# Performance work log

Measured on AMD Instinct MI355X. Metric: run time of the kernel, lower is better.

## Reference

```python
import jax, jax.numpy as jnp
import numpy as np

B = 8192; L = 68; NPG = L + 1; N = B * NPG
IN = 4; HID = 64; OUT = 7; NL = 8
BN_EPS = 1e-5


def setup_inputs() -> dict:
    key = jax.random.key(0)
    ks = jax.random.split(key, 12)
    # graph topology (same for every graph): ring among L landmarks + master node (idx L)
    # connected to every landmark; directed edges both ways (PyG-style edge_index).
    ring = np.stack([np.arange(L), (np.arange(L) + 1) % L])            # [2, L]
    mast = np.stack([np.arange(L), np.full(L, L)])                     # [2, L]
    und = np.concatenate([ring, mast], axis=1)                         # [2, 2L]
    e = np.concatenate([und, und[::-1]], axis=1)                       # [2, 4L]
    offs = (np.arange(B) * NPG)[:, None, None]
    edge_index = (e[None] + offs).transpose(1, 0, 2).reshape(2, -1)    # [2, B*4L]
    s = 1.0 / np.sqrt(HID)
    return {
        "x": jax.random.normal(ks[0], (N, IN), jnp.float32),
        "edge_index": jnp.asarray(edge_index, jnp.int32),
        "batch": jnp.repeat(jnp.arange(B, dtype=jnp.int32), NPG),
        "master_mask": jnp.tile(jnp.arange(NPG) == L, B),
        "conv_first_W": jax.random.normal(ks[1], (IN, HID), jnp.float32) * 0.5,
        "conv_first_b": jnp.zeros((HID,), jnp.float32),
        "conv_mid_W": jax.random.normal(ks[2], (NL - 2, HID, HID), jnp.float32) * s,
        "conv_mid_b": jnp.zeros((NL - 2, HID), jnp.float32),
        "conv_last_W": jax.random.normal(ks[3], (HID, HID), jnp.float32) * s,
        "conv_last_b": jnp.zeros((HID,), jnp.float32),
        "bn_gamma": jnp.ones((NL - 1, HID), jnp.float32),
        "bn_beta": jnp.zeros((NL - 1, HID), jnp.float32),
        "bn_mean": jax.random.normal(ks[4], (NL - 1, HID), jnp.float32) * 0.1,
        "bn_var": jax.random.uniform(ks[5], (NL - 1, HID), jnp.float32) * 0.5 + 0.5,
        "att_W1": jax.random.normal(ks[6], (HID, HID), jnp.float32) * s,
        "att_b1": jnp.zeros((HID,), jnp.float32),
        "att_W2": jax.random.normal(ks[7], (HID, 1), jnp.float32) * s,
        "att_b2": jnp.zeros((1,), jnp.float32),
        "fc1_W": jax.random.normal(ks[8], (3 * HID, HID), jnp.float32) / np.sqrt(3 * HID),
        "fc1_b": jnp.zeros((HID,), jnp.float32),
        "fc2_W": jax.random.normal(ks[9], (HID, OUT), jnp.float32) * s,
        "fc2_b": jnp.zeros((OUT,), jnp.float32),
    }


def reference(x, edge_index, batch, master_mask,
              conv_first_W, conv_first_b, conv_mid_W, conv_mid_b,
              conv_last_W, conv_last_b, bn_gamma, bn_beta, bn_mean, bn_var,
              att_W1, att_b1, att_W2, att_b2, fc1_W, fc1_b, fc2_W, fc2_b):
    n = x.shape[0]
    src, dst = edge_index[0], edge_index[1]
    # GCN symmetric normalization with self-loops: deg_i = 1 + in-degree
    deg = 1.0 + jax.ops.segment_sum(jnp.ones_like(src, x.dtype), dst, num_segments=n)
    dis = jax.lax.rsqrt(deg)
    enorm = (dis[src] * dis[dst])[:, None]                 # [E,1]
    self_norm = (1.0 / deg)[:, None]                       # [N,1] self-loop coeff

    def gcn(h, W, b):
        h = h @ W                                          # [N,HID]
        agg = jax.ops.segment_sum(h[src] * enorm, dst, num_segments=n)
        return agg + h * self_norm + b

    def bn(h, i):  # eval-mode BatchNorm1d
        return bn_gamma[i] * (h - bn_mean[i]) * jax.lax.rsqrt(bn_var[i] + BN_EPS) + bn_beta[i]

    h = bn(jax.nn.relu(gcn(x, conv_first_W, conv_first_b)), 0)
    for i in range(NL - 2):  # residual GCN blocks
        h = bn(jax.nn.relu(gcn(h, conv_mid_W[i], conv_mid_b[i])), i + 1) + h
    h = jax.nn.relu(gcn(h, conv_last_W, conv_last_b))

    mfl = master_mask.astype(h.dtype)                      # [N]
    mcnt = jax.ops.segment_sum(mfl, batch, num_segments=B)
    master = jax.ops.segment_sum(h * mfl[:, None], batch, num_segments=B) / mcnt[:, None]
    att = jax.nn.sigmoid(jax.nn.relu(master @ att_W1 + att_b1) @ att_W2 + att_b2)
    master = master * att

    rfl = 1.0 - mfl
    rcnt = jax.ops.segment_sum(rfl, batch, num_segments=B)
    x_mean = jax.ops.segment_sum(h * rfl[:, None], batch, num_segments=B) / rcnt[:, None]
    h_masked = jnp.where(master_mask[:, None], -jnp.inf, h)
    x_max = jax.ops.segment_max(h_masked, batch, num_segments=B)

    g = jnp.concatenate([x_mean, x_max, master], axis=1)   # [B, 3*HID]
    return jax.nn.relu(g @ fc1_W + fc1_b) @ fc2_W + fc2_b  # [B, OUT]
```

## Files before the change

### kernel.cpp

```cpp
#include <hip/hip_runtime.h>

typedef float f32x4 __attribute__((ext_vector_type(4)));
typedef short short8 __attribute__((ext_vector_type(8)));
typedef unsigned int u32;
typedef unsigned short u16;

#define CLL 0.25f
#define CML 0.06019292654288460f
#define SELFM 0.014492753623188406f

__device__ __forceinline__ u16 f2bf(float x) {
  u32 b = __float_as_uint(x);
  return (u16)((b + 0x7FFFu + ((b >> 16) & 1u)) >> 16);
}
__device__ __forceinline__ u32 cvtpk(float a, float b) {
  u32 r;
  asm("v_cvt_pk_bf16_f32 %0, %1, %2" : "=v"(r) : "v"(a), "v"(b));
  return r;
}

__global__ void prep(const float* __restrict__ midW, const float* __restrict__ lastW,
                     const float* __restrict__ bng, const float* __restrict__ bnb,
                     const float* __restrict__ bnm, const float* __restrict__ bnv,
                     u16* __restrict__ frag, float* __restrict__ bns) {
  const int t0 = blockIdx.x * blockDim.x + threadIdx.x;
  for (int u = t0; u < 7 * 4 * 2 * 64; u += gridDim.x * blockDim.x) {
    const int lane = u & 63;
    const int t = u >> 6;
    const int ks = t & 1;
    const int nt = (t >> 1) & 3;
    const int l = t >> 3;
    const float* W = (l < 6) ? (midW + l * 4096) : lastW;
    const int col = nt * 16 + (lane & 15);
    const int kb = ks * 32 + (lane >> 4) * 8;
    u16* dst = frag + (size_t)u * 8;
#pragma unroll
    for (int j = 0; j < 8; ++j) dst[j] = f2bf(W[(kb + j) * 64 + col]);
  }
  for (int u = t0; u < 7 * 64; u += gridDim.x * blockDim.x) {
    const int l = u >> 6, f = u & 63;
    const float sc = (float)((double)bng[l * 64 + f] / sqrt((double)bnv[l * 64 + f] + 1e-5));
    bns[l * 128 + f] = sc;
    bns[l * 128 + 64 + f] = bnb[l * 64 + f] - bnm[l * 64 + f] * sc;
  }
}

#define SUM4(V) ((V)[0] + (V)[1] + (V)[2] + (V)[3])
#define MAX4(V) fmaxf(fmaxf((V)[0], (V)[1]), fmaxf((V)[2], (V)[3]))

#define STEP2(MT, TA, TPA, TNA, TB, TPB, TNB, HA, HB, RESID)           \
  {                                                                    \
    const float spA_ = (qg == 3) ? TPA[3] : TA[3];                     \
    const float spB_ = (qg == 3) ? TPB[3] : TB[3];                     \
    const u32 pvP_ = (u32)__shfl((int)cvtpk(spA_, spB_), (lane + 48) & 63, 64); \
    const float snA_ = (qg == 0) ? TNA[0] : TA[0];                     \
    const float snB_ = (qg == 0) ? TNB[0] : TB[0];                     \
    const u32 nvP_ = (u32)__shfl((int)cvtpk(snA_, snB_), (lane + 16) & 63, 64); \
    const float pvA_ = __uint_as_float(pvP_ << 16);                    \
    const float pvB_ = __uint_as_float(pvP_ & 0xffff0000u);            \
    const float nvA_ = __uint_as_float(nvP_ << 16);                    \
    const float nvB_ = __uint_as_float(nvP_ & 0xffff0000u);            \
    const float ta0A_ = ((MT) == 0 && qg == 0) ? tA4[3] : pvA_;        \
    const float ta0B_ = ((MT) == 0 && qg == 0) ? tB4[3] : pvB_;        \
    const float tb3A_ = ((MT) == 4 && qg == 0) ? tA0[0] : nvA_;        \
    const float tb3B_ = ((MT) == 4 && qg == 0) ? tB0[0] : nvB_;        \
    float oA0 = fmaf(CLL, ta0A_ + TA[0] + TA[1], cmtA_);               \
    float oA1 = fmaf(CLL, TA[0] + TA[1] + TA[2], cmtA_);               \
    float oA2 = fmaf(CLL, TA[1] + TA[2] + TA[3], cmtA_);               \
    float oA3 = fmaf(CLL, TA[2] + TA[3] + tb3A_, cmtA_);               \
    float oB0 = fmaf(CLL, ta0B_ + TB[0] + TB[1], cmtB_);               \
    float oB1 = fmaf(CLL, TB[0] + TB[1] + TB[2], cmtB_);               \
    float oB2 = fmaf(CLL, TB[1] + TB[2] + TB[3], cmtB_);               \
    float oB3 = fmaf(CLL, TB[2] + TB[3] + tb3B_, cmtB_);               \
    oA0 = fmaf(fmaxf(oA0, 0.f), scA_, shA_);                           \
    oA1 = fmaf(fmaxf(oA1, 0.f), scA_, shA_);                           \
    oA2 = fmaf(fmaxf(oA2, 0.f), scA_, shA_);                           \
    oA3 = fmaf(fmaxf(oA3, 0.f), scA_, shA_);                           \
    oB0 = fmaf(fmaxf(oB0, 0.f), scB_, shB_);                           \
    oB1 = fmaf(fmaxf(oB1, 0.f), scB_, shB_);                           \
    oB2 = fmaf(fmaxf(oB2, 0.f), scB_, shB_);                           \
    oB3 = fmaf(fmaxf(oB3, 0.f), scB_, shB_);                           \
    if (RESID) {                                                       \
      oA0 += HA[0]; oA1 += HA[1]; oA2 += HA[2]; oA3 += HA[3];          \
      oB0 += HB[0]; oB1 += HB[1]; oB2 += HB[2]; oB3 += HB[3];          \
    }                                                                  \
    HA[0] = oA0; HA[1] = oA1; HA[2] = oA2; HA[3] = oA3;                \
    HB[0] = oB0; HB[1] = oB1; HB[2] = oB2; HB[3] = oB3;                \
  }

#define WPAIR2(HW, MT, H, CQ)                                          \
  {                                                                    \
    const u32 pa = cvtpk(H[0], H[1]);                                  \
    const u32 pb = cvtpk(H[2], H[3]);                                  \
    (HW)[(16 * (MT) + 4 * qg + 0) * 64 + (CQ)] = (u16)pa;              \
    (HW)[(16 * (MT) + 4 * qg + 1) * 64 + ((CQ) ^ 8)] = (u16)(pa >> 16);\
    (HW)[(16 * (MT) + 4 * qg + 2) * 64 + ((CQ) ^ 16)] = (u16)pb;       \
    (HW)[(16 * (MT) + 4 * qg + 3) * 64 + ((CQ) ^ 24)] = (u16)(pb >> 16); \
  }

#define EPILOG2(RESID, WRITE, HBW, BA, BB, SCA, SHA, SCB, SHB)         \
  {                                                                    \
    float SA_ = SUM4(tA0) + SUM4(tA1) + SUM4(tA2) + SUM4(tA3) + SUM4(tA4); \
    float SB_ = SUM4(tB0) + SUM4(tB1) + SUM4(tB2) + SUM4(tB3) + SUM4(tB4); \
    if (qg == 1) { SA_ -= tA4[0]; SB_ -= tB4[0]; }                     \
    SA_ += __shfl_xor(SA_, 16, 64);                                    \
    SA_ += __shfl_xor(SA_, 32, 64);                                    \
    SB_ += __shfl_xor(SB_, 16, 64);                                    \
    SB_ += __shfl_xor(SB_, 32, 64);                                    \
    const u32 pk_ = (u32)__shfl((int)cvtpk(tA4[0], tB4[0]), 16 + p15, 64); \
    const float scA_ = (SCA), shA_ = (SHA), scB_ = (SCB), shB_ = (SHB);\
    const float cmtA_ = fmaf(CML, __uint_as_float(pk_ << 16), (BA));   \
    const float cmtB_ = fmaf(CML, __uint_as_float(pk_ & 0xffff0000u), (BB)); \
    float mvA_ = 0.f, mvB_ = 0.f;                                      \
    if (qg == 1) {                                                     \
      mvA_ = fmaf(fmaxf(fmaf(CML, SA_, fmaf(SELFM, tA4[0], (BA))), 0.f), scA_, shA_); \
      mvB_ = fmaf(fmaxf(fmaf(CML, SB_, fmaf(SELFM, tB4[0], (BB))), 0.f), scB_, shB_); \
      if (RESID) { mvA_ += hA4[0]; mvB_ += hB4[0]; }                   \
    }                                                                  \
    STEP2(0, tA0, tA4, tA1, tB0, tB4, tB1, hA0, hB0, RESID)            \
    STEP2(1, tA1, tA0, tA2, tB1, tB0, tB2, hA1, hB1, RESID)            \
    STEP2(2, tA2, tA1, tA3, tB2, tB1, tB3, hA2, hB2, RESID)            \
    STEP2(3, tA3, tA2, tA4, tB3, tB2, tB4, hA3, hB3, RESID)            \
    STEP2(4, tA4, tA3, tA0, tB4, tB3, tB0, hA4, hB4, RESID)            \
    if (qg == 1) { hA4[0] = mvA_; hB4[0] = mvB_; }                     \
    if (WRITE) {                                                       \
      u16* hw_ = (HBW);                                                \
      WPAIR2(hw_, 0, hA0, cqA) WPAIR2(hw_, 0, hB0, cqB)                \
      WPAIR2(hw_, 1, hA1, cqA) WPAIR2(hw_, 1, hB1, cqB)                \
      WPAIR2(hw_, 2, hA2, cqA) WPAIR2(hw_, 2, hB2, cqB)                \
      WPAIR2(hw_, 3, hA3, cqA) WPAIR2(hw_, 3, hB3, cqB)                \
      if (qg == 0) { WPAIR2(hw_, 4, hA4, cqA) WPAIR2(hw_, 4, hB4, cqB) } \
      else if (qg == 1) {                                              \
        hw_[68 * 64 + (cA ^ 32)] = (u16)cvtpk(mvA_, mvA_);             \
        hw_[68 * 64 + (cB ^ 32)] = (u16)cvtpk(mvB_, mvB_);             \
      }                                                                \
    }                                                                  \
  }

#define MM(A, B, C) __builtin_amdgcn_mfma_f32_16x16x32_bf16(A, B, C, 0, 0, 0)

#define MP3(HR, MT, TA, TB)                                            \
  {                                                                    \
    const short8 a0 = *(const short8*)&(HR)[(MT) * 1024 + ra0];        \
    const short8 a1 = *(const short8*)&(HR)[(MT) * 1024 + ra1];        \
    f32x4 accA = z4, accB = z4;                                        \
    accA = MM(a0, bA0, accA); accA = MM(a1, bA1, accA);                \
    accB = MM(a0, bB0, accB); accB = MM(a1, bB1, accB);                \
    TA = accA; TB = accB;                                              \
  }

__launch_bounds__(128)
__global__ void gcn_fused(
    const float* __restrict__ x,
    const float* __restrict__ cfW, const float* __restrict__ cfb,
    const float* __restrict__ cmb, const float* __restrict__ clb,
    const float* __restrict__ aW1, const float* __restrict__ ab1,
    const float* __restrict__ aW2, const float* __restrict__ ab2,
    const float* __restrict__ f1W, const float* __restrict__ f1b,
    const float* __restrict__ f2W, const float* __restrict__ f2b,
    const u16* __restrict__ frag, const float* __restrict__ bns,
    float* __restrict__ out) {
  __shared__ u16 hb[2][80 * 64];
  __shared__ float xl4[80 * 4];
  __shared__ float mrow[64];
  __shared__ float gv[192];
  __shared__ float part[128];

  const int tid = threadIdx.x;
  const int g = blockIdx.x;
  const int lane = tid & 63;
  const int w = tid >> 6;
  const int p15 = lane & 15;
  const int qg = lane >> 4;
  const int cA = w * 32 + p15;
  const int cB = cA + 16;
  const f32x4 z4 = {0.f, 0.f, 0.f, 0.f};

  const int rsw = (p15 & 7) << 3;
  const int ra0 = (p15 * 64 + qg * 8) ^ rsw;
  const int ra1 = (p15 * 64 + 32 + qg * 8) ^ rsw;
  const int cqA = cA ^ ((qg & 1) << 5);
  const int cqB = cqA ^ 16;

  const u16* f0p = frag + (((size_t)(2 * w) * 2) * 64 + lane) * 8;
  const u16* f1p = frag + (((size_t)(2 * w + 1) * 2) * 64 + lane) * 8;
  short8 bA0 = *(const short8*)f0p;
  short8 bA1 = *(const short8*)(f0p + 512);
  short8 bB0 = *(const short8*)f1p;
  short8 bB1 = *(const short8*)(f1p + 512);

  {
    u32* hz = (u32*)hb;
#pragma unroll
    for (int it = 0; it < 3; ++it) {
      const int i = tid + it * 128;
      if (i < 352) {
        hz[2208 + i] = 0u;
        hz[2560 + 2208 + i] = 0u;
      }
    }
  }
  if (tid < 69)
    *(f32x4*)&xl4[tid * 4] = *(const f32x4*)&x[((size_t)g * 69 + tid) * 4];
  else if (tid < 80)
    *(f32x4*)&xl4[tid * 4] = z4;

  f32x4 tA0, tA1, tA2, tA3, tA4, tB0, tB1, tB2, tB3, tB4;
  f32x4 hA0, hA1, hA2, hA3, hA4, hB0, hB1, hB2, hB3, hB4;

  __syncthreads();

  {
    const float wA0 = cfW[cA], wA1 = cfW[64 + cA], wA2 = cfW[128 + cA], wA3 = cfW[192 + cA];
    const float wB0 = cfW[cB], wB1 = cfW[64 + cB], wB2 = cfW[128 + cB], wB3 = cfW[192 + cB];
#define L0T(MT, TA, TB)                                                \
    { _Pragma("unroll") for (int r = 0; r < 4; ++r) {                  \
        const f32x4 xv = *(const f32x4*)&xl4[(16 * (MT) + 4 * qg + r) * 4]; \
        TA[r] = fmaf(xv[0], wA0, fmaf(xv[1], wA1, fmaf(xv[2], wA2, xv[3] * wA3))); \
        TB[r] = fmaf(xv[0], wB0, fmaf(xv[1], wB1, fmaf(xv[2], wB2, xv[3] * wB3))); } }
    L0T(0, tA0, tB0) L0T(1, tA1, tB1) L0T(2, tA2, tB2) L0T(3, tA3, tB3) L0T(4, tA4, tB4)
#undef L0T
  }
  EPILOG2(false, true, &hb[0][0], cfb[cA], cfb[cB], bns[cA], bns[64 + cA],
          bns[cB], bns[64 + cB])
  __syncthreads();

#pragma unroll 1
  for (int l = 1; l <= 6; ++l) {
    const u16* fA = frag + ((((size_t)l * 4 + 2 * w) * 2) * 64 + lane) * 8;
    const u16* fB = frag + ((((size_t)l * 4 + 2 * w + 1) * 2) * 64 + lane) * 8;
    const short8 nA0 = *(const short8*)fA;
    const short8 nA1 = *(const short8*)(fA + 512);
    const short8 nB0 = *(const short8*)fB;
    const short8 nB1 = *(const short8*)(fB + 512);
    const float biasA = cmb[(l - 1) * 64 + cA];
    const float biasB = cmb[(l - 1) * 64 + cB];
    const float lscA = bns[l * 128 + cA], lshA = bns[l * 128 + 64 + cA];
    const float lscB = bns[l * 128 + cB], lshB = bns[l * 128 + 64 + cB];
    const u16* hr = &hb[(l + 1) & 1][0];
    MP3(hr, 0, tA0, tB0) MP3(hr, 1, tA1, tB1) MP3(hr, 2, tA2, tB2)
    MP3(hr, 3, tA3, tB3) MP3(hr, 4, tA4, tB4)
    bA0 = nA0; bA1 = nA1; bB0 = nB0; bB1 = nB1;
    EPILOG2(true, true, &hb[l & 1][0], biasA, biasB, lscA, lshA, lscB, lshB)
    __syncthreads();
  }

  {
    const u16* hr = &hb[0][0];
    MP3(hr, 0, tA0, tB0) MP3(hr, 1, tA1, tB1) MP3(hr, 2, tA2, tB2)
    MP3(hr, 3, tA3, tB3) MP3(hr, 4, tA4, tB4)
    EPILOG2(false, false, (u16*)nullptr, clb[cA], clb[cB], 1.f, 0.f, 1.f, 0.f)
  }

  {
    float sA = SUM4(hA0) + SUM4(hA1) + SUM4(hA2) + SUM4(hA3);
    float sB = SUM4(hB0) + SUM4(hB1) + SUM4(hB2) + SUM4(hB3);
    float mA = fmaxf(fmaxf(MAX4(hA0), MAX4(hA1)), fmaxf(MAX4(hA2), MAX4(hA3)));
    float mB = fmaxf(fmaxf(MAX4(hB0), MAX4(hB1)), fmaxf(MAX4(hB2), MAX4(hB3)));
    if (qg == 0) {
      sA += SUM4(hA4); mA = fmaxf(mA, MAX4(hA4));
      sB += SUM4(hB4); mB = fmaxf(mB, MAX4(hB4));
    }
    sA += __shfl_xor(sA, 16, 64); sA += __shfl_xor(sA, 32, 64);
    sB += __shfl_xor(sB, 16, 64); sB += __shfl_xor(sB, 32, 64);
    mA = fmaxf(mA, __shfl_xor(mA, 16, 64)); mA = fmaxf(mA, __shfl_xor(mA, 32, 64));
    mB = fmaxf(mB, __shfl_xor(mB, 16, 64)); mB = fmaxf(mB, __shfl_xor(mB, 32, 64));
    if (qg == 0) {
      gv[cA] = sA * (1.f / 68.f);
      gv[64 + cA] = mA;
      gv[cB] = sB * (1.f / 68.f);
      gv[64 + cB] = mB;
    }
    if (qg == 1) { mrow[cA] = hA4[0]; mrow[cB] = hB4[0]; }
  }
  __syncthreads();

  {
    const int f = tid & 63;
    const int kh = tid >> 6;
    float z = 0.f;
#pragma unroll
    for (int k = 0; k < 32; ++k)
      z = fmaf(mrow[kh * 32 + k], aW1[(kh * 32 + k) * 64 + f], z);
    part[tid] = z;
  }
  __syncthreads();
  if (tid < 64) {
    float z = part[tid] + part[64 + tid] + ab1[tid];
    z = fmaxf(z, 0.f);
    float pr = z * aW2[tid];
#pragma unroll
    for (int off = 32; off > 0; off >>= 1) pr += __shfl_xor(pr, off, 64);
    const float att = 1.f / (1.f + expf(-(pr + ab2[0])));
    gv[128 + tid] = mrow[tid] * att;
  }
  __syncthreads();

  {
    const int f = tid & 63;
    const int ih = tid >> 6;
    float a = 0.f;
#pragma unroll
    for (int i = 0; i < 96; ++i)
      a = fmaf(gv[ih * 96 + i], f1W[(ih * 96 + i) * 64 + f], a);
    part[tid] = a;
  }
  __syncthreads();
  if (tid < 64) {
    float a = part[tid] + part[64 + tid] + f1b[tid];
    const float y = fmaxf(a, 0.f);
    float po[7];
#pragma unroll
    for (int o = 0; o < 7; ++o) po[o] = y * f2W[tid * 7 + o];
#pragma unroll
    for (int o = 0; o < 7; ++o)
#pragma unroll
      for (int off = 32; off > 0; off >>= 1) po[o] += __shfl_xor(po[o], off, 64);
    if (tid == 0) {
#pragma unroll
      for (int o = 0; o < 7; ++o) out[(size_t)g * 7 + o] = po[o] + f2b[o];
    }
  }
}

extern "C" void kernel_launch(void* const* d_in, const int* in_sizes, int n_in,
                              void* d_out, int out_size, void* d_ws, size_t ws_size,
                              hipStream_t stream) {
  (void)in_sizes; (void)n_in; (void)ws_size;
  const float* x   = (const float*)d_in[0];
  const float* cfW = (const float*)d_in[4];
  const float* cfb = (const float*)d_in[5];
  const float* cmW = (const float*)d_in[6];
  const float* cmb = (const float*)d_in[7];
  const float* clW = (const float*)d_in[8];
  const float* clb = (const float*)d_in[9];
  const float* bng = (const float*)d_in[10];
  const float* bnb = (const float*)d_in[11];
  const float* bnm = (const float*)d_in[12];
  const float* bnv = (const float*)d_in[13];
  const float* aW1 = (const float*)d_in[14];
  const float* ab1 = (const float*)d_in[15];
  const float* aW2 = (const float*)d_in[16];
  const float* ab2 = (const float*)d_in[17];
  const float* f1W = (const float*)d_in[18];
  const float* f1b = (const float*)d_in[19];
  const float* f2W = (const float*)d_in[20];
  const float* f2b = (const float*)d_in[21];

  u16* frag = (u16*)d_ws;
  float* bns = (float*)((char*)d_ws + 57344);
  const int ngraphs = out_size / 7;

  prep<<<dim3(16), dim3(256), 0, stream>>>(cmW, clW, bng, bnb, bnm, bnv, frag, bns);
  gcn_fused<<<dim3(ngraphs), dim3(128), 0, stream>>>(
      x, cfW, cfb, cmb, clb, aW1, ab1, aW2, ab2, f1W, f1b, f2W, f2b,
      frag, bns, (float*)d_out);
}
```

Baseline: 157.0 us.

## Move graph aggregation to MFMA with constant adjacency fragments and fold BN scale into weights

Replaces the shuffle-based ring/master neighbour aggregation epilogue with a second MFMA pass. Transformed features are written to a transposed LDS buffer and multiplied by a precomputed bf16 normalized-adjacency matrix, with the bias folded in as an extra column. BatchNorm scale is folded into the weights and biases in the prep kernel, so the epilogue is just relu plus shift plus residual. This cuts VALU and cross-lane shuffle work but adds LDS round-trips, 12 resident fragment registers, and extra bf16 rounding of the intermediate and bias values.

```diff
diff --git a/kernel.cpp b/kernel.cpp
--- a/kernel.cpp
+++ b/kernel.cpp
@@ -4,10 +4,12 @@
 typedef short short8 __attribute__((ext_vector_type(8)));
 typedef unsigned int u32;
 typedef unsigned short u16;
+typedef u32 u32x2 __attribute__((ext_vector_type(2)));
 
 #define CLL 0.25f
 #define CML 0.06019292654288460f
 #define SELFM 0.014492753623188406f
+#define UCS 208
 
 __device__ __forceinline__ u16 f2bf(float x) {
   u32 b = __float_as_uint(x);
@@ -22,70 +24,117 @@
 __global__ void prep(const float* __restrict__ midW, const float* __restrict__ lastW,
                      const float* __restrict__ bng, const float* __restrict__ bnb,
                      const float* __restrict__ bnm, const float* __restrict__ bnv,
-                     u16* __restrict__ frag, float* __restrict__ bns) {
+                     const float* __restrict__ cfb, const float* __restrict__ cmb,
+                     const float* __restrict__ clb,
+                     u16* __restrict__ frag, float* __restrict__ bns,
+                     u16* __restrict__ afr, u16* __restrict__ bb) {
   const int t0 = blockIdx.x * blockDim.x + threadIdx.x;
-  for (int u = t0; u < 7 * 4 * 2 * 64; u += gridDim.x * blockDim.x) {
+  const int stride = gridDim.x * blockDim.x;
+  for (int u = t0; u < 7 * 64; u += stride) {
+    const int l = u >> 6, f = u & 63;
+    const float sc = (float)((double)bng[l * 64 + f] / sqrt((double)bnv[l * 64 + f] + 1e-5));
+    bns[l * 128 + f] = sc;
+    bns[l * 128 + 64 + f] = bnb[l * 64 + f] - bnm[l * 64 + f] * sc;
+  }
+  for (int u = t0; u < 7 * 4 * 2 * 64; u += stride) {
     const int lane = u & 63;
     const int t = u >> 6;
     const int ks = t & 1;
     const int nt = (t >> 1) & 3;
-    const int l = t >> 3;
-    const float* W = (l < 6) ? (midW + l * 4096) : lastW;
+    const int lf = t >> 3;
+    const float* W = (lf < 6) ? (midW + lf * 4096) : lastW;
     const int col = nt * 16 + (lane & 15);
     const int kb = ks * 32 + (lane >> 4) * 8;
+    float scale = 1.f;
+    if (lf < 6)
+      scale = (float)((double)bng[(lf + 1) * 64 + col] /
+                      sqrt((double)bnv[(lf + 1) * 64 + col] + 1e-5));
     u16* dst = frag + (size_t)u * 8;
 #pragma unroll
-    for (int j = 0; j < 8; ++j) dst[j] = f2bf(W[(kb + j) * 64 + col]);
-  }
-  for (int u = t0; u < 7 * 64; u += gridDim.x * blockDim.x) {
-    const int l = u >> 6, f = u & 63;
-    const float sc = (float)((double)bng[l * 64 + f] / sqrt((double)bnv[l * 64 + f] + 1e-5));
-    bns[l * 128 + f] = sc;
-    bns[l * 128 + 64 + f] = bnb[l * 64 + f] - bnm[l * 64 + f] * sc;
+    for (int j = 0; j < 8; ++j) dst[j] = f2bf(W[(kb + j) * 64 + col] * scale);
+  }
+  for (int u = t0; u < 8 * 64; u += stride) {
+    const int l = u >> 6, c = u & 63;
+    float b, s = 1.f;
+    if (l == 0) {
+      b = cfb[c];
+      s = (float)((double)bng[c] / sqrt((double)bnv[c] + 1e-5));
+    } else if (l <= 6) {
+      b = cmb[(l - 1) * 64 + c];
+      s = (float)((double)bng[l * 64 + c] / sqrt((double)bnv[l * 64 + c] + 1e-5));
+    } else {
+      b = clb[c];
+    }
+    bb[l * 64 + c] = f2bf(b * s);
+  }
+  const int MTs[12] = {0, 1, 2, 4, 1, 2, 3, 4, 0, 1, 3, 4};
+  const int KSs[12] = {0, 0, 0, 0, 1, 1, 1, 1, 2, 2, 2, 2};
+  for (int u = t0; u < 12 * 64; u += stride) {
+    const int p = u >> 6, lane = u & 63;
+    const int r = MTs[p] * 16 + (lane & 15);
+    const int kb = KSs[p] * 32 + ((lane >> 4) << 3);
+    u16* dst = afr + (size_t)u * 8;
+#pragma unroll
+    for (int j = 0; j < 8; ++j) {
+      const int k = kb + j;
+      float v = 0.f;
+      if (r < 68) {
+        if (k < 68) {
+          if (k == r || k == (r + 1) % 68 || k == (r + 67) % 68) v = CLL;
+        } else if (k == 68) v = CML;
+        else if (k == 80) v = 1.f;
+      } else if (r == 68) {
+        if (k < 68) v = CML;
+        else if (k == 68) v = SELFM;
+        else if (k == 80) v = 1.f;
+      }
+      dst[j] = f2bf(v);
+    }
   }
 }
 
 #define SUM4(V) ((V)[0] + (V)[1] + (V)[2] + (V)[3])
 #define MAX4(V) fmaxf(fmaxf((V)[0], (V)[1]), fmaxf((V)[2], (V)[3]))
-
-#define STEP2(MT, TA, TPA, TNA, TB, TPB, TNB, HA, HB, RESID)           \
-  {                                                                    \
-    const float spA_ = (qg == 3) ? TPA[3] : TA[3];                     \
-    const float spB_ = (qg == 3) ? TPB[3] : TB[3];                     \
-    const u32 pvP_ = (u32)__shfl((int)cvtpk(spA_, spB_), (lane + 48) & 63, 64); \
-    const float snA_ = (qg == 0) ? TNA[0] : TA[0];                     \
-    const float snB_ = (qg == 0) ? TNB[0] : TB[0];                     \
-    const u32 nvP_ = (u32)__shfl((int)cvtpk(snA_, snB_), (lane + 16) & 63, 64); \
-    const float pvA_ = __uint_as_float(pvP_ << 16);                    \
-    const float pvB_ = __uint_as_float(pvP_ & 0xffff0000u);            \
-    const float nvA_ = __uint_as_float(nvP_ << 16);                    \
-    const float nvB_ = __uint_as_float(nvP_ & 0xffff0000u);            \
-    const float ta0A_ = ((MT) == 0 && qg == 0) ? tA4[3] : pvA_;        \
-    const float ta0B_ = ((MT) == 0 && qg == 0) ? tB4[3] : pvB_;        \
-    const float tb3A_ = ((MT) == 4 && qg == 0) ? tA0[0] : nvA_;        \
-    const float tb3B_ = ((MT) == 4 && qg == 0) ? tB0[0] : nvB_;        \
-    float oA0 = fmaf(CLL, ta0A_ + TA[0] + TA[1], cmtA_);               \
-    float oA1 = fmaf(CLL, TA[0] + TA[1] + TA[2], cmtA_);               \
-    float oA2 = fmaf(CLL, TA[1] + TA[2] + TA[3], cmtA_);               \
-    float oA3 = fmaf(CLL, TA[2] + TA[3] + tb3A_, cmtA_);               \
-    float oB0 = fmaf(CLL, ta0B_ + TB[0] + TB[1], cmtB_);               \
-    float oB1 = fmaf(CLL, TB[0] + TB[1] + TB[2], cmtB_);               \
-    float oB2 = fmaf(CLL, TB[1] + TB[2] + TB[3], cmtB_);               \
-    float oB3 = fmaf(CLL, TB[2] + TB[3] + tb3B_, cmtB_);               \
-    oA0 = fmaf(fmaxf(oA0, 0.f), scA_, shA_);                           \
-    oA1 = fmaf(fmaxf(oA1, 0.f), scA_, shA_);                           \
-    oA2 = fmaf(fmaxf(oA2, 0.f), scA_, shA_);                           \
-    oA3 = fmaf(fmaxf(oA3, 0.f), scA_, shA_);                           \
-    oB0 = fmaf(fmaxf(oB0, 0.f), scB_, shB_);                           \
-    oB1 = fmaf(fmaxf(oB1, 0.f), scB_, shB_);                           \
-    oB2 = fmaf(fmaxf(oB2, 0.f), scB_, shB_);                           \
-    oB3 = fmaf(fmaxf(oB3, 0.f), scB_, shB_);                           \
-    if (RESID) {                                                       \
-      oA0 += HA[0]; oA1 += HA[1]; oA2 += HA[2]; oA3 += HA[3];          \
-      oB0 += HB[0]; oB1 += HB[1]; oB2 += HB[2]; oB3 += HB[3];          \
+#define MM(A, B, C) __builtin_amdgcn_mfma_f32_16x16x32_bf16(A, B, C, 0, 0, 0)
+
+#define MP3(HR, MT, TA, TB)                                            \
+  {                                                                    \
+    const short8 a0 = *(const short8*)&(HR)[(MT) * 1024 + ra0];        \
+    const short8 a1 = *(const short8*)&(HR)[(MT) * 1024 + ra1];        \
+    f32x4 accA = z4, accB = z4;                                        \
+    accA = MM(a0, bA0, accA); accA = MM(a1, bA1, accA);                \
+    accB = MM(a0, bB0, accB); accB = MM(a1, bB1, accB);                \
+    TA = accA; TB = accB;                                              \
+  }
+
+#define UW2(MT, TA, TB)                                                \
+  {                                                                    \
+    u32x2 wa, wb;                                                      \
+    wa.x = cvtpk(TA[0], TA[1]); wa.y = cvtpk(TA[2], TA[3]);            \
+    wb.x = cvtpk(TB[0], TB[1]); wb.y = cvtpk(TB[2], TB[3]);            \
+    *(u32x2*)((char*)ucm + uwA + 32 * (MT)) = wa;                      \
+    *(u32x2*)((char*)ucm + uwB + 32 * (MT)) = wb;                      \
+  }
+
+#define AGG5(URB, AG0, AG1, AG2, AG3, AG4)                             \
+  {                                                                    \
+    const short8 ub0 = *(const short8*)((const char*)ucm + (URB));       \
+    const short8 ub1 = *(const short8*)((const char*)ucm + (URB) + 64);  \
+    const short8 ub2 = *(const short8*)((const char*)ucm + (URB) + 128); \
+    AG0 = MM(F8, ub2, MM(F0, ub0, z4));                                \
+    AG1 = MM(F9, ub2, MM(F4, ub1, MM(F1, ub0, z4)));                   \
+    AG2 = MM(F9, ub2, MM(F5, ub1, MM(F2, ub0, z4)));                   \
+    AG3 = MM(F10, ub2, MM(F6, ub1, z4));                               \
+    AG4 = MM(F11, ub2, MM(F7, ub1, MM(F3, ub0, z4)));                  \
+  }
+
+#define EPI4(AG, H, SH, RESID)                                         \
+  {                                                                    \
+    _Pragma("unroll") for (int e = 0; e < 4; ++e) {                    \
+      float v = fmaxf(AG[e], 0.f) + (SH);                              \
+      if (RESID) v += H[e];                                            \
+      H[e] = v;                                                        \
     }                                                                  \
-    HA[0] = oA0; HA[1] = oA1; HA[2] = oA2; HA[3] = oA3;                \
-    HB[0] = oB0; HB[1] = oB1; HB[2] = oB2; HB[3] = oB3;                \
   }
 
 #define WPAIR2(HW, MT, H, CQ)                                          \
@@ -98,69 +147,32 @@
     (HW)[(16 * (MT) + 4 * qg + 3) * 64 + ((CQ) ^ 24)] = (u16)(pb >> 16); \
   }
 
-#define EPILOG2(RESID, WRITE, HBW, BA, BB, SCA, SHA, SCB, SHB)         \
-  {                                                                    \
-    float SA_ = SUM4(tA0) + SUM4(tA1) + SUM4(tA2) + SUM4(tA3) + SUM4(tA4); \
-    float SB_ = SUM4(tB0) + SUM4(tB1) + SUM4(tB2) + SUM4(tB3) + SUM4(tB4); \
-    if (qg == 1) { SA_ -= tA4[0]; SB_ -= tB4[0]; }                     \
-    SA_ += __shfl_xor(SA_, 16, 64);                                    \
-    SA_ += __shfl_xor(SA_, 32, 64);                                    \
-    SB_ += __shfl_xor(SB_, 16, 64);                                    \
-    SB_ += __shfl_xor(SB_, 32, 64);                                    \
-    const u32 pk_ = (u32)__shfl((int)cvtpk(tA4[0], tB4[0]), 16 + p15, 64); \
-    const float scA_ = (SCA), shA_ = (SHA), scB_ = (SCB), shB_ = (SHB);\
-    const float cmtA_ = fmaf(CML, __uint_as_float(pk_ << 16), (BA));   \
-    const float cmtB_ = fmaf(CML, __uint_as_float(pk_ & 0xffff0000u), (BB)); \
-    float mvA_ = 0.f, mvB_ = 0.f;                                      \
-    if (qg == 1) {                                                     \
-      mvA_ = fmaf(fmaxf(fmaf(CML, SA_, fmaf(SELFM, tA4[0], (BA))), 0.f), scA_, shA_); \
-      mvB_ = fmaf(fmaxf(fmaf(CML, SB_, fmaf(SELFM, tB4[0], (BB))), 0.f), scB_, shB_); \
-      if (RESID) { mvA_ += hA4[0]; mvB_ += hB4[0]; }                   \
+#define HWRITE(HW)                                                     \
+  {                                                                    \
+    u16* hw_ = (HW);                                                   \
+    WPAIR2(hw_, 0, hA0, cqA) WPAIR2(hw_, 0, hB0, cqB)                  \
+    WPAIR2(hw_, 1, hA1, cqA) WPAIR2(hw_, 1, hB1, cqB)                  \
+    WPAIR2(hw_, 2, hA2, cqA) WPAIR2(hw_, 2, hB2, cqB)                  \
+    WPAIR2(hw_, 3, hA3, cqA) WPAIR2(hw_, 3, hB3, cqB)                  \
+    if (qg == 0) { WPAIR2(hw_, 4, hA4, cqA) WPAIR2(hw_, 4, hB4, cqB) } \
+    else if (qg == 1) {                                                \
+      hw_[68 * 64 + (cA ^ 32)] = (u16)cvtpk(hA4[0], hA4[0]);           \
+      hw_[68 * 64 + (cB ^ 32)] = (u16)cvtpk(hB4[0], hB4[0]);           \
     }                                                                  \
-    STEP2(0, tA0, tA4, tA1, tB0, tB4, tB1, hA0, hB0, RESID)            \
-    STEP2(1, tA1, tA0, tA2, tB1, tB0, tB2, hA1, hB1, RESID)            \
-    STEP2(2, tA2, tA1, tA3, tB2, tB1, tB3, hA2, hB2, RESID)            \
-    STEP2(3, tA3, tA2, tA4, tB3, tB2, tB4, hA3, hB3, RESID)            \
-    STEP2(4, tA4, tA3, tA0, tB4, tB3, tB0, hA4, hB4, RESID)            \
-    if (qg == 1) { hA4[0] = mvA_; hB4[0] = mvB_; }                     \
-    if (WRITE) {                                                       \
-      u16* hw_ = (HBW);                                                \
-      WPAIR2(hw_, 0, hA0, cqA) WPAIR2(hw_, 0, hB0, cqB)                \
-      WPAIR2(hw_, 1, hA1, cqA) WPAIR2(hw_, 1, hB1, cqB)                \
-      WPAIR2(hw_, 2, hA2, cqA) WPAIR2(hw_, 2, hB2, cqB)                \
-      WPAIR2(hw_, 3, hA3, cqA) WPAIR2(hw_, 3, hB3, cqB)                \
-      if (qg == 0) { WPAIR2(hw_, 4, hA4, cqA) WPAIR2(hw_, 4, hB4, cqB) } \
-      else if (qg == 1) {                                              \
-        hw_[68 * 64 + (cA ^ 32)] = (u16)cvtpk(mvA_, mvA_);             \
-        hw_[68 * 64 + (cB ^ 32)] = (u16)cvtpk(mvB_, mvB_);             \
-      }                                                                \
-    }                                                                  \
-  }
-
-#define MM(A, B, C) __builtin_amdgcn_mfma_f32_16x16x32_bf16(A, B, C, 0, 0, 0)
-
-#define MP3(HR, MT, TA, TB)                                            \
-  {                                                                    \
-    const short8 a0 = *(const short8*)&(HR)[(MT) * 1024 + ra0];        \
-    const short8 a1 = *(const short8*)&(HR)[(MT) * 1024 + ra1];        \
-    f32x4 accA = z4, accB = z4;                                        \
-    accA = MM(a0, bA0, accA); accA = MM(a1, bA1, accA);                \
-    accB = MM(a0, bB0, accB); accB = MM(a1, bB1, accB);                \
-    TA = accA; TB = accB;                                              \
   }
 
 __launch_bounds__(128)
 __global__ void gcn_fused(
-    const float* __restrict__ x,
-    const float* __restrict__ cfW, const float* __restrict__ cfb,
-    const float* __restrict__ cmb, const float* __restrict__ clb,
+    const float* __restrict__ x, const float* __restrict__ cfW,
     const float* __restrict__ aW1, const float* __restrict__ ab1,
     const float* __restrict__ aW2, const float* __restrict__ ab2,
     const float* __restrict__ f1W, const float* __restrict__ f1b,
     const float* __restrict__ f2W, const float* __restrict__ f2b,
     const u16* __restrict__ frag, const float* __restrict__ bns,
+    const u16* __restrict__ afr, const u16* __restrict__ bb,
     float* __restrict__ out) {
   __shared__ u16 hb[2][80 * 64];
+  __shared__ __align__(16) u16 ucm[64 * (UCS / 2)];
   __shared__ float xl4[80 * 4];
   __shared__ float mrow[64];
   __shared__ float gv[192];
@@ -172,7 +184,7 @@
   const int w = tid >> 6;
   const int p15 = lane & 15;
   const int qg = lane >> 4;
-  const int cA = w * 32 + p15;
+  const int cA = 32 * w + p15;
   const int cB = cA + 16;
   const f32x4 z4 = {0.f, 0.f, 0.f, 0.f};
 
@@ -181,6 +193,24 @@
   const int ra1 = (p15 * 64 + 32 + qg * 8) ^ rsw;
   const int cqA = cA ^ ((qg & 1) << 5);
   const int cqB = cqA ^ 16;
+  const int uwA = cA * UCS + 8 * qg;
+  const int uwB = cB * UCS + 8 * qg;
+  const int urA = cA * UCS + 16 * qg;
+  const int urB = cB * UCS + 16 * qg;
+
+  const u16* ap = afr + (size_t)lane * 8;
+  const short8 F0 = *(const short8*)(ap);
+  const short8 F1 = *(const short8*)(ap + 512);
+  const short8 F2 = *(const short8*)(ap + 1024);
+  const short8 F3 = *(const short8*)(ap + 1536);
+  const short8 F4 = *(const short8*)(ap + 2048);
+  const short8 F5 = *(const short8*)(ap + 2560);
+  const short8 F6 = *(const short8*)(ap + 3072);
+  const short8 F7 = *(const short8*)(ap + 3584);
+  const short8 F8 = *(const short8*)(ap + 4096);
+  const short8 F9 = *(const short8*)(ap + 4608);
+  const short8 F10 = *(const short8*)(ap + 5120);
+  const short8 F11 = *(const short8*)(ap + 5632);
 
   const u16* f0p = frag + (((size_t)(2 * w) * 2) * 64 + lane) * 8;
   const u16* f1p = frag + (((size_t)(2 * w + 1) * 2) * 64 + lane) * 8;
@@ -199,6 +229,9 @@
         hz[2560 + 2208 + i] = 0u;
       }
     }
+    const int col = tid >> 1, half = tid & 1;
+    *(f32x4*)((char*)ucm + col * UCS + 160 + 16 * half) = z4;
+    if (half == 0) *(f32x4*)((char*)ucm + col * UCS + 192) = z4;
   }
   if (tid < 69)
     *(f32x4*)&xl4[tid * 4] = *(const f32x4*)&x[((size_t)g * 69 + tid) * 4];
@@ -211,8 +244,11 @@
   __syncthreads();
 
   {
-    const float wA0 = cfW[cA], wA1 = cfW[64 + cA], wA2 = cfW[128 + cA], wA3 = cfW[192 + cA];
-    const float wB0 = cfW[cB], wB1 = cfW[64 + cB], wB2 = cfW[128 + cB], wB3 = cfW[192 + cB];
+    const float sA = bns[cA], sB = bns[cB];
+    const float wA0 = cfW[cA] * sA, wA1 = cfW[64 + cA] * sA;
+    const float wA2 = cfW[128 + cA] * sA, wA3 = cfW[192 + cA] * sA;
+    const float wB0 = cfW[cB] * sB, wB1 = cfW[64 + cB] * sB;
+    const float wB2 = cfW[128 + cB] * sB, wB3 = cfW[192 + cB] * sB;
 #define L0T(MT, TA, TB)                                                \
     { _Pragma("unroll") for (int r = 0; r < 4; ++r) {                  \
         const f32x4 xv = *(const f32x4*)&xl4[(16 * (MT) + 4 * qg + r) * 4]; \
@@ -220,9 +256,21 @@
         TB[r] = fmaf(xv[0], wB0, fmaf(xv[1], wB1, fmaf(xv[2], wB2, xv[3] * wB3))); } }
     L0T(0, tA0, tB0) L0T(1, tA1, tB1) L0T(2, tA2, tB2) L0T(3, tA3, tB3) L0T(4, tA4, tB4)
 #undef L0T
-  }
-  EPILOG2(false, true, &hb[0][0], cfb[cA], cfb[cB], bns[cA], bns[64 + cA],
-          bns[cB], bns[64 + cB])
+    UW2(0, tA0, tB0) UW2(1, tA1, tB1) UW2(2, tA2, tB2) UW2(3, tA3, tB3) UW2(4, tA4, tB4)
+    if (qg == 0) {
+      ucm[cA * (UCS / 2) + 80] = bb[cA];
+      ucm[cB * (UCS / 2) + 80] = bb[cB];
+    }
+    const float shA = bns[64 + cA], shB = bns[64 + cB];
+    f32x4 gA0, gA1, gA2, gA3, gA4, gB0, gB1, gB2, gB3, gB4;
+    AGG5(urA, gA0, gA1, gA2, gA3, gA4)
+    AGG5(urB, gB0, gB1, gB2, gB3, gB4)
+    EPI4(gA0, hA0, shA, false) EPI4(gA1, hA1, shA, false) EPI4(gA2, hA2, shA, false)
+    EPI4(gA3, hA3, shA, false) EPI4(gA4, hA4, shA, false)
+    EPI4(gB0, hB0, shB, false) EPI4(gB1, hB1, shB, false) EPI4(gB2, hB2, shB, false)
+    EPI4(gB3, hB3, shB, false) EPI4(gB4, hB4, shB, false)
+    HWRITE(&hb[0][0])
+  }
   __syncthreads();
 
 #pragma unroll 1
@@ -233,15 +281,25 @@
     const short8 nA1 = *(const short8*)(fA + 512);
     const short8 nB0 = *(const short8*)fB;
     const short8 nB1 = *(const short8*)(fB + 512);
-    const float biasA = cmb[(l - 1) * 64 + cA];
-    const float biasB = cmb[(l - 1) * 64 + cB];
-    const float lscA = bns[l * 128 + cA], lshA = bns[l * 128 + 64 + cA];
-    const float lscB = bns[l * 128 + cB], lshB = bns[l * 128 + 64 + cB];
+    const float shA = bns[l * 128 + 64 + cA], shB = bns[l * 128 + 64 + cB];
+    const u16 brA = bb[l * 64 + cA], brB = bb[l * 64 + cB];
     const u16* hr = &hb[(l + 1) & 1][0];
     MP3(hr, 0, tA0, tB0) MP3(hr, 1, tA1, tB1) MP3(hr, 2, tA2, tB2)
     MP3(hr, 3, tA3, tB3) MP3(hr, 4, tA4, tB4)
     bA0 = nA0; bA1 = nA1; bB0 = nB0; bB1 = nB1;
-    EPILOG2(true, true, &hb[l & 1][0], biasA, biasB, lscA, lshA, lscB, lshB)
+    UW2(0, tA0, tB0) UW2(1, tA1, tB1) UW2(2, tA2, tB2) UW2(3, tA3, tB3) UW2(4, tA4, tB4)
+    if (qg == 0) {
+      ucm[cA * (UCS / 2) + 80] = brA;
+      ucm[cB * (UCS / 2) + 80] = brB;
+    }
+    f32x4 gA0, gA1, gA2, gA3, gA4, gB0, gB1, gB2, gB3, gB4;
+    AGG5(urA, gA0, gA1, gA2, gA3, gA4)
+    AGG5(urB, gB0, gB1, gB2, gB3, gB4)
+    EPI4(gA0, hA0, shA, true) EPI4(gA1, hA1, shA, true) EPI4(gA2, hA2, shA, true)
+    EPI4(gA3, hA3, shA, true) EPI4(gA4, hA4, shA, true)
+    EPI4(gB0, hB0, shB, true) EPI4(gB1, hB1, shB, true) EPI4(gB2, hB2, shB, true)
+    EPI4(gB3, hB3, shB, true) EPI4(gB4, hB4, shB, true)
+    HWRITE(&hb[l & 1][0])
     __syncthreads();
   }
 
@@ -249,7 +307,18 @@
     const u16* hr = &hb[0][0];
     MP3(hr, 0, tA0, tB0) MP3(hr, 1, tA1, tB1) MP3(hr, 2, tA2, tB2)
     MP3(hr, 3, tA3, tB3) MP3(hr, 4, tA4, tB4)
-    EPILOG2(false, false, (u16*)nullptr, clb[cA], clb[cB], 1.f, 0.f, 1.f, 0.f)
+    UW2(0, tA0, tB0) UW2(1, tA1, tB1) UW2(2, tA2, tB2) UW2(3, tA3, tB3) UW2(4, tA4, tB4)
+    if (qg == 0) {
+      ucm[cA * (UCS / 2) + 80] = bb[7 * 64 + cA];
+      ucm[cB * (UCS / 2) + 80] = bb[7 * 64 + cB];
+    }
+    f32x4 gA0, gA1, gA2, gA3, gA4, gB0, gB1, gB2, gB3, gB4;
+    AGG5(urA, gA0, gA1, gA2, gA3, gA4)
+    AGG5(urB, gB0, gB1, gB2, gB3, gB4)
+    EPI4(gA0, hA0, 0.f, false) EPI4(gA1, hA1, 0.f, false) EPI4(gA2, hA2, 0.f, false)
+    EPI4(gA3, hA3, 0.f, false) EPI4(gA4, hA4, 0.f, false)
+    EPI4(gB0, hB0, 0.f, false) EPI4(gB1, hB1, 0.f, false) EPI4(gB2, hB2, 0.f, false)
+    EPI4(gB3, hB3, 0.f, false) EPI4(gB4, hB4, 0.f, false)
   }
 
   {
@@ -347,12 +416,15 @@
   const float* f2W = (const float*)d_in[20];
   const float* f2b = (const float*)d_in[21];
 
-  u16* frag = (u16*)d_ws;
+  u16* frag  = (u16*)d_ws;
   float* bns = (float*)((char*)d_ws + 57344);
+  u16* afr   = (u16*)((char*)d_ws + 60928);
+  u16* bb    = (u16*)((char*)d_ws + 73216);
   const int ngraphs = out_size / 7;
 
-  prep<<<dim3(16), dim3(256), 0, stream>>>(cmW, clW, bng, bnb, bnm, bnv, frag, bns);
+  prep<<<dim3(16), dim3(256), 0, stream>>>(cmW, clW, bng, bnb, bnm, bnv,
+                                           cfb, cmb, clb, frag, bns, afr, bb);
   gcn_fused<<<dim3(ngraphs), dim3(128), 0, stream>>>(
-      x, cfW, cfb, cmb, clb, aW1, ab1, aW2, ab2, f1W, f1b, f2W, f2b,
-      frag, bns, (float*)d_out);
+      x, cfW, aW1, ab1, aW2, ab2, f1W, f1b, f2W, f2b,
+      frag, bns, afr, bb, (float*)d_out);
 }
```

After: 163.8 us. +4.3%, slower.
